# Kernel optimization log

Hardware: AMD Instinct MI355X
Metric: run time of the kernel (lower is better)

Reference implementation:

```python
import jax, jax.numpy as jnp
import numpy as np

N, M, E, C_IN, C_OUT = 100000, 20000, 1600000, 128, 128


def _safe_inv(d):
    # 1/d with 0 where d==0 (matches PyG D[D==inf]=0), grad-safe
    safe = jnp.where(d > 0, d, 1.0)
    return jnp.where(d > 0, 1.0 / safe, 0.0)


def _hconv(x, node_idx, edge_idx, hw, W, b):
    # PyG HypergraphConv, use_attention=False, heads=1:
    # X' = D^{-1} H B^{-1} H^T (X Theta) + bias, D uses hyperedge_weight
    xt = x @ W  # [N, C_OUT]
    D = jax.ops.segment_sum(hw[edge_idx], node_idx, num_segments=N)
    Dinv = _safe_inv(D)  # [N]
    Bc = jax.ops.segment_sum(jnp.ones((E,), dtype=x.dtype), edge_idx, num_segments=M)
    Binv = _safe_inv(Bc)  # [M]
    # node -> hyperedge (message weighted by B^{-1} of target edge)
    e = jax.ops.segment_sum(Binv[edge_idx][:, None] * xt[node_idx], edge_idx, num_segments=M)
    # hyperedge -> node (message weighted by D^{-1} of target node)
    out = jax.ops.segment_sum(Dinv[node_idx][:, None] * e[edge_idx], node_idx, num_segments=N)
    return out + b


def setup_inputs() -> dict:
    key = jax.random.key(0)
    ks = jax.random.split(key, 12)
    x = jax.random.normal(ks[0], (N, C_IN), dtype=jnp.float32)
    node_idx = jax.random.randint(ks[1], (E,), 0, N, dtype=jnp.int32)
    edge_idx = jax.random.randint(ks[2], (E,), 0, M, dtype=jnp.int32)
    hyperedge_index = jnp.stack([node_idx, edge_idx])
    hyperedge_weight = jax.random.uniform(ks[3], (M,), dtype=jnp.float32) + 0.5
    hyperedge_attr = jax.random.normal(ks[4], (M, C_IN), dtype=jnp.float32)
    batch = jnp.zeros((N,), dtype=jnp.int32)
    s1 = 1.0 / np.sqrt(C_IN)
    s2 = 1.0 / np.sqrt(C_OUT)
    W1 = jax.random.uniform(ks[5], (C_IN, C_OUT), minval=-s1, maxval=s1, dtype=jnp.float32)
    W2 = jax.random.uniform(ks[6], (C_OUT, C_OUT), minval=-s2, maxval=s2, dtype=jnp.float32)
    W3 = jax.random.uniform(ks[7], (C_OUT, C_OUT), minval=-s2, maxval=s2, dtype=jnp.float32)
    b1 = jax.random.uniform(ks[8], (C_OUT,), minval=-s1, maxval=s1, dtype=jnp.float32)
    b2 = jax.random.uniform(ks[9], (C_OUT,), minval=-s2, maxval=s2, dtype=jnp.float32)
    b3 = jax.random.uniform(ks[10], (C_OUT,), minval=-s2, maxval=s2, dtype=jnp.float32)
    return {"x": x, "hyperedge_index": hyperedge_index, "hyperedge_weight": hyperedge_weight,
            "hyperedge_attr": hyperedge_attr, "batch": batch,
            "W1": W1, "b1": b1, "W2": W2, "b2": b2, "W3": W3, "b3": b3}


def reference(x, hyperedge_index, hyperedge_weight, hyperedge_attr, batch,
              W1, b1, W2, b2, W3, b3):
    node_idx = hyperedge_index[0]
    edge_idx = hyperedge_index[1]
    # dropout is identity in eval mode; hyperedge_attr/batch unused (no attention)
    h = jax.nn.relu(_hconv(x, node_idx, edge_idx, hyperedge_weight, W1, b1))
    h = jax.nn.relu(_hconv(h, node_idx, edge_idx, hyperedge_weight, W2, b2))
    h = jax.nn.relu(_hconv(h, node_idx, edge_idx, hyperedge_weight, W3, b3))
    return h
```

## Files before the change

kernel.cpp:

```cpp
#include <hip/hip_runtime.h>
#include <hip/hip_fp16.h>

#define NN 100000
#define MM 20000
#define EE 1600000

#define NBLK_E 256
#define CHUNK_E (EE / NBLK_E)
#define NBLK_N 128
#define CHUNK_N (EE / NBLK_N)
#define NRANGE 25000

#define SCAN_BLOCK 256
#define SCAN_ITEMS 8
#define SCAN_TILE (SCAN_BLOCK * SCAN_ITEMS)
#define NB_E ((MM + SCAN_TILE - 1) / SCAN_TILE)
#define NB_N ((NN + SCAN_TILE - 1) / SCAN_TILE)
#define NB_TOT (NB_E + NB_N)

static inline size_t align256(size_t x) { return (x + 255) & ~(size_t)255; }

struct alignas(8) half4 { __half2 lo, hi; };

__device__ __forceinline__ float4 h4_to_f4(half4 v) {
  float2 a = __half22float2(v.lo);
  float2 b = __half22float2(v.hi);
  return make_float4(a.x, a.y, b.x, b.y);
}
__device__ __forceinline__ half4 f4_to_h4(float4 v) {
  half4 r;
  r.lo = __float22half2_rn(make_float2(v.x, v.y));
  r.hi = __float22half2_rn(make_float2(v.z, v.w));
  return r;
}

__global__ __launch_bounds__(256) void cvt_f2h_kernel(
    const float* __restrict__ in, __half* __restrict__ out, int n4) {
  int i = blockIdx.x * 256 + threadIdx.x;
  int stride = gridDim.x * 256;
  for (; i < n4; i += stride) {
    float4 v = ((const float4*)in)[i];
    ((half4*)out)[i] = f4_to_h4(v);
  }
}

__global__ __launch_bounds__(256) void ehist_kernel(
    const int* __restrict__ edge_idx,
    int* __restrict__ bcnt_e, unsigned short* __restrict__ lrank_e) {
  extern __shared__ int hist[];
  int b = blockIdx.x;
  for (int k = threadIdx.x; k < MM; k += 256) hist[k] = 0;
  __syncthreads();
  int lo = b * CHUNK_E, hi = lo + CHUNK_E;
  for (int i = lo + threadIdx.x; i < hi; i += 256) {
    int e = edge_idx[i];
    int r = atomicAdd(&hist[e], 1);
    lrank_e[i] = (unsigned short)r;
  }
  __syncthreads();
  int* row = bcnt_e + (size_t)b * MM;
  for (int k = threadIdx.x; k < MM; k += 256) row[k] = hist[k];
}

__global__ __launch_bounds__(256) void nhist_kernel(
    const int* __restrict__ node_idx,
    int* __restrict__ bcnt_n, unsigned short* __restrict__ lrank_n) {
  extern __shared__ int hist[];
  int b = blockIdx.x;
  int lo = b * CHUNK_N, hi = lo + CHUNK_N;
  int* row = bcnt_n + (size_t)b * NN;
  for (int p = 0; p < 4; ++p) {
    int base = p * NRANGE;
    for (int k = threadIdx.x; k < NRANGE; k += 256) hist[k] = 0;
    __syncthreads();
    for (int i = lo + threadIdx.x; i < hi; i += 256) {
      int n = node_idx[i] - base;
      if ((unsigned)n < (unsigned)NRANGE) {
        int r = atomicAdd(&hist[n], 1);
        lrank_n[i] = (unsigned short)r;
      }
    }
    __syncthreads();
    for (int k = threadIdx.x; k < NRANGE; k += 256) row[base + k] = hist[k];
    __syncthreads();
  }
}

__global__ __launch_bounds__(256) void colscan_e_kernel(
    int* __restrict__ bcnt_e, int* __restrict__ ecnt) {
  int e = blockIdx.x * 256 + threadIdx.x;
  if (e >= MM) return;
  int run = 0;
#pragma unroll 8
  for (int b = 0; b < NBLK_E; ++b) {
    size_t idx = (size_t)b * MM + e;
    int v = bcnt_e[idx];
    bcnt_e[idx] = run;
    run += v;
  }
  ecnt[e] = run;
}

__global__ __launch_bounds__(256) void colscan_n_kernel(
    int* __restrict__ bcnt_n, int* __restrict__ ncnt) {
  int n = blockIdx.x * 256 + threadIdx.x;
  if (n >= NN) return;
  int run = 0;
#pragma unroll 8
  for (int b = 0; b < NBLK_N; ++b) {
    size_t idx = (size_t)b * NN + n;
    int v = bcnt_n[idx];
    bcnt_n[idx] = run;
    run += v;
  }
  ncnt[n] = run;
}

__global__ __launch_bounds__(SCAN_BLOCK) void scan_partial_kernel(
    const int* __restrict__ ecnt, const int* __restrict__ ncnt,
    int* __restrict__ eptr, int* __restrict__ nptr, int* __restrict__ bsum) {
  __shared__ int lds[SCAN_BLOCK];
  int b = blockIdx.x;
  const int* cnt; int* ptr; int len; int lb;
  if (b < NB_E) { cnt = ecnt; ptr = eptr; len = MM; lb = b; }
  else          { cnt = ncnt; ptr = nptr; len = NN; lb = b - NB_E; }
  int t = threadIdx.x;
  int lo = lb * SCAN_TILE + t * SCAN_ITEMS;
  int v[SCAN_ITEMS];
  int s = 0;
#pragma unroll
  for (int j = 0; j < SCAN_ITEMS; ++j) {
    int idx = lo + j;
    v[j] = (idx < len) ? cnt[idx] : 0;
    s += v[j];
  }
  lds[t] = s;
  __syncthreads();
  for (int d = 1; d < SCAN_BLOCK; d <<= 1) {
    int o = (t >= d) ? lds[t - d] : 0;
    __syncthreads();
    lds[t] += o;
    __syncthreads();
  }
  int run = lds[t] - s;
#pragma unroll
  for (int j = 0; j < SCAN_ITEMS; ++j) {
    int idx = lo + j;
    if (idx < len) ptr[idx] = run;
    run += v[j];
  }
  if (t == SCAN_BLOCK - 1) bsum[b] = lds[t];
}

__global__ void scan_bsum_kernel(int* __restrict__ bsum) {
  int t = threadIdx.x;
  if (t == 0) {
    int run = 0;
    for (int i = 0; i < NB_E; ++i) { int c = bsum[i]; bsum[i] = run; run += c; }
  } else if (t == 1) {
    int run = 0;
    for (int i = NB_E; i < NB_TOT; ++i) { int c = bsum[i]; bsum[i] = run; run += c; }
  }
}

__global__ __launch_bounds__(SCAN_BLOCK) void scan_fixup_kernel(
    int* __restrict__ eptr, int* __restrict__ nptr,
    const int* __restrict__ ecnt, const int* __restrict__ bsum,
    float* __restrict__ Binv) {
  int b = blockIdx.x;
  int* ptr; int len; int lb; bool isE;
  if (b < NB_E) { ptr = eptr; len = MM; lb = b; isE = true; }
  else          { ptr = nptr; len = NN; lb = b - NB_E; isE = false; }
  int boff = bsum[b];
  int t = threadIdx.x;
  int lo = lb * SCAN_TILE + t * SCAN_ITEMS;
#pragma unroll
  for (int j = 0; j < SCAN_ITEMS; ++j) {
    int idx = lo + j;
    if (idx < len) {
      ptr[idx] += boff;
      if (isE) {
        int c = ecnt[idx];
        Binv[idx] = (c > 0) ? 1.0f / (float)c : 0.0f;
      }
    }
  }
  if (b == 0 && t == 0) { eptr[MM] = EE; nptr[NN] = EE; }
}

__global__ __launch_bounds__(256) void fill2_kernel(
    const int* __restrict__ node_idx, const int* __restrict__ edge_idx,
    const int* __restrict__ eptr, const int* __restrict__ nptr,
    const int* __restrict__ bcnt_e, const int* __restrict__ bcnt_n,
    const unsigned short* __restrict__ lrank_e,
    const unsigned short* __restrict__ lrank_n,
    int* __restrict__ edge_nodes, int* __restrict__ node_edges) {
  int i = blockIdx.x * 256 + threadIdx.x;
  if (i >= EE) return;
  int e = edge_idx[i];
  int n = node_idx[i];
  int be = i / CHUNK_E;
  int bn = i / CHUNK_N;
  int slotE = eptr[e] + bcnt_e[(size_t)be * MM + e] + (int)lrank_e[i];
  edge_nodes[slotE] = n;
  int slotN = nptr[n] + bcnt_n[(size_t)bn * NN + n] + (int)lrank_n[i];
  node_edges[slotN] = e;
}

__global__ __launch_bounds__(256) void dinv_csr_kernel(
    const int* __restrict__ nptr, const int* __restrict__ node_edges,
    const float* __restrict__ hw, float* __restrict__ Dinv) {
  int n = blockIdx.x * 256 + threadIdx.x;
  if (n >= NN) return;
  int lo = nptr[n], hi = nptr[n + 1];
  float d = 0.0f;
  for (int j = lo; j < hi; ++j) d += hw[node_edges[j]];
  Dinv[n] = (d > 0.0f) ? 1.0f / d : 0.0f;
}

__device__ __forceinline__ void fma4(float4& acc, float s, const float4& m) {
  acc.x += s * m.x;
  acc.y += s * m.y;
  acc.z += s * m.z;
  acc.w += s * m.w;
}

__global__ __launch_bounds__(256) void gemm128_kernel(
    const __half* __restrict__ X, const float* __restrict__ W,
    __half* __restrict__ Y, int nrows) {
  __shared__ float Wl[128 * 128];
  float4* Wl4 = (float4*)Wl;
  const float4* W4 = (const float4*)W;
  for (int i = threadIdx.x; i < 128 * 32; i += 256) Wl4[i] = W4[i];
  __syncthreads();

  int tc = threadIdx.x & 15;
  int tr = threadIdx.x >> 4;
  int base = blockIdx.x * 64;
  int r[4];
  bool v[4];
#pragma unroll
  for (int j = 0; j < 4; ++j) {
    int rr = base + tr + j * 16;
    v[j] = rr < nrows;
    r[j] = v[j] ? rr : 0;
  }
  float4 acc[4][2];
#pragma unroll
  for (int j = 0; j < 4; ++j) {
    acc[j][0] = make_float4(0.f, 0.f, 0.f, 0.f);
    acc[j][1] = make_float4(0.f, 0.f, 0.f, 0.f);
  }
#pragma unroll 4
  for (int k4 = 0; k4 < 32; ++k4) {
    float4 xv[4];
#pragma unroll
    for (int j = 0; j < 4; ++j)
      xv[j] = h4_to_f4(((const half4*)X)[(size_t)r[j] * 32 + k4]);
#pragma unroll
    for (int kk = 0; kk < 4; ++kk) {
      float4 wva = Wl4[(k4 * 4 + kk) * 32 + tc];
      float4 wvb = Wl4[(k4 * 4 + kk) * 32 + 16 + tc];
#pragma unroll
      for (int j = 0; j < 4; ++j) {
        float xk = ((const float*)&xv[j])[kk];
        fma4(acc[j][0], xk, wva);
        fma4(acc[j][1], xk, wvb);
      }
    }
  }
#pragma unroll
  for (int j = 0; j < 4; ++j) {
    if (v[j]) {
      ((half4*)Y)[(size_t)r[j] * 32 + tc] = f4_to_h4(acc[j][0]);
      ((half4*)Y)[(size_t)r[j] * 32 + 16 + tc] = f4_to_h4(acc[j][1]);
    }
  }
}

__global__ __launch_bounds__(256) void edge_agg_kernel(
    const __half* __restrict__ hin, const int* __restrict__ eptr,
    const int* __restrict__ edge_nodes, const float* __restrict__ Binv,
    __half* __restrict__ eout) {
  int half_id = threadIdx.x >> 5;
  int lane = threadIdx.x & 31;
  int m = blockIdx.x * 8 + half_id;
  if (m >= MM) return;
  int lo = eptr[m], hi = eptr[m + 1];
  const half4* h4p = (const half4*)hin;
  float4 acc = make_float4(0.f, 0.f, 0.f, 0.f);
  int j = lo;
  for (; j + 4 <= hi; j += 4) {
    int n0 = edge_nodes[j + 0];
    int n1 = edge_nodes[j + 1];
    int n2 = edge_nodes[j + 2];
    int n3 = edge_nodes[j + 3];
    float4 a = h4_to_f4(h4p[(size_t)n0 * 32 + lane]);
    float4 b = h4_to_f4(h4p[(size_t)n1 * 32 + lane]);
    float4 c = h4_to_f4(h4p[(size_t)n2 * 32 + lane]);
    float4 d = h4_to_f4(h4p[(size_t)n3 * 32 + lane]);
    acc.x += (a.x + b.x) + (c.x + d.x);
    acc.y += (a.y + b.y) + (c.y + d.y);
    acc.z += (a.z + b.z) + (c.z + d.z);
    acc.w += (a.w + b.w) + (c.w + d.w);
  }
  for (; j < hi; ++j) {
    int n = edge_nodes[j];
    float4 a = h4_to_f4(h4p[(size_t)n * 32 + lane]);
    acc.x += a.x; acc.y += a.y; acc.z += a.z; acc.w += a.w;
  }
  float bi = Binv[m];
  acc.x *= bi; acc.y *= bi; acc.z *= bi; acc.w *= bi;
  ((half4*)eout)[(size_t)m * 32 + lane] = f4_to_h4(acc);
}

__device__ __forceinline__ void strow(float* Y, size_t i, float4 v) {
  ((float4*)Y)[i] = v;
}
__device__ __forceinline__ void strow(__half* Y, size_t i, float4 v) {
  ((half4*)Y)[i] = f4_to_h4(v);
}

template <typename TOUT>
__global__ __launch_bounds__(256) void node_agg_kernel(
    const __half* __restrict__ ein, const int* __restrict__ nptr,
    const int* __restrict__ node_edges, const float* __restrict__ Dinv,
    const float* __restrict__ bias, TOUT* __restrict__ out) {
  int half_id = threadIdx.x >> 5;
  int lane = threadIdx.x & 31;
  int n = blockIdx.x * 8 + half_id;
  if (n >= NN) return;
  int lo = nptr[n], hi = nptr[n + 1];
  const half4* e4 = (const half4*)ein;
  float4 acc = make_float4(0.f, 0.f, 0.f, 0.f);
  int j = lo;
  for (; j + 4 <= hi; j += 4) {
    int m0 = node_edges[j + 0];
    int m1 = node_edges[j + 1];
    int m2 = node_edges[j + 2];
    int m3 = node_edges[j + 3];
    float4 a = h4_to_f4(e4[(size_t)m0 * 32 + lane]);
    float4 b = h4_to_f4(e4[(size_t)m1 * 32 + lane]);
    float4 c = h4_to_f4(e4[(size_t)m2 * 32 + lane]);
    float4 d = h4_to_f4(e4[(size_t)m3 * 32 + lane]);
    acc.x += (a.x + b.x) + (c.x + d.x);
    acc.y += (a.y + b.y) + (c.y + d.y);
    acc.z += (a.z + b.z) + (c.z + d.z);
    acc.w += (a.w + b.w) + (c.w + d.w);
  }
  for (; j < hi; ++j) {
    int m = node_edges[j];
    float4 a = h4_to_f4(e4[(size_t)m * 32 + lane]);
    acc.x += a.x; acc.y += a.y; acc.z += a.z; acc.w += a.w;
  }
  float di = Dinv[n];
  float4 bb = ((const float4*)bias)[lane];
  float4 rv;
  rv.x = fmaxf(di * acc.x + bb.x, 0.f);
  rv.y = fmaxf(di * acc.y + bb.y, 0.f);
  rv.z = fmaxf(di * acc.z + bb.z, 0.f);
  rv.w = fmaxf(di * acc.w + bb.w, 0.f);
  strow(out, (size_t)n * 32 + lane, rv);
}

extern "C" void kernel_launch(void* const* d_in, const int* in_sizes, int n_in,
                              void* d_out, int out_size, void* d_ws, size_t ws_size,
                              hipStream_t stream) {
  const float* x = (const float*)d_in[0];
  const int* hidx = (const int*)d_in[1];
  const int* node_idx = hidx;
  const int* edge_idx = hidx + EE;
  const float* hw = (const float*)d_in[2];
  const float* W1 = (const float*)d_in[5];
  const float* b1 = (const float*)d_in[6];
  const float* W2 = (const float*)d_in[7];
  const float* b2 = (const float*)d_in[8];
  const float* W3 = (const float*)d_in[9];
  const float* b3 = (const float*)d_in[10];
  float* out = (float*)d_out;

  char* ws = (char*)d_ws;
  size_t off = 0;
  auto alloc = [&](size_t bytes) -> char* {
    char* p = ws + off;
    off = align256(off + bytes);
    return p;
  };
  __half* xh   = (__half*)alloc(sizeof(__half) * (size_t)NN * 128);
  __half* h    = (__half*)alloc(sizeof(__half) * (size_t)NN * 128);
  __half* eraw = (__half*)alloc(sizeof(__half) * (size_t)MM * 128);
  __half* et   = (__half*)alloc(sizeof(__half) * (size_t)MM * 128);
  int*   bcnt_e = (int*)alloc(sizeof(int) * (size_t)NBLK_E * MM);
  int*   bcnt_n = (int*)alloc(sizeof(int) * (size_t)NBLK_N * NN);
  unsigned short* lrank_e = (unsigned short*)alloc(sizeof(short) * (size_t)EE);
  unsigned short* lrank_n = (unsigned short*)alloc(sizeof(short) * (size_t)EE);
  int*   ecnt  = (int*)alloc(sizeof(int) * MM);
  int*   ncnt  = (int*)alloc(sizeof(int) * NN);
  int*   eptr  = (int*)alloc(sizeof(int) * (MM + 1));
  int*   nptr  = (int*)alloc(sizeof(int) * (NN + 1));
  int*   bsum  = (int*)alloc(sizeof(int) * NB_TOT);
  float* Binv  = (float*)alloc(sizeof(float) * MM);
  float* Dinv  = (float*)alloc(sizeof(float) * NN);
  int* edge_nodes = (int*)alloc(sizeof(int) * (size_t)EE);
  int* node_edges = (int*)alloc(sizeof(int) * (size_t)EE);
  (void)ws_size; (void)in_sizes; (void)n_in; (void)out_size;

  ehist_kernel<<<NBLK_E, 256, MM * sizeof(int), stream>>>(edge_idx, bcnt_e, lrank_e);
  nhist_kernel<<<NBLK_N, 256, NRANGE * sizeof(int), stream>>>(node_idx, bcnt_n, lrank_n);
  colscan_e_kernel<<<(MM + 255) / 256, 256, 0, stream>>>(bcnt_e, ecnt);
  colscan_n_kernel<<<(NN + 255) / 256, 256, 0, stream>>>(bcnt_n, ncnt);
  scan_partial_kernel<<<NB_TOT, SCAN_BLOCK, 0, stream>>>(ecnt, ncnt, eptr, nptr, bsum);
  scan_bsum_kernel<<<1, 64, 0, stream>>>(bsum);
  scan_fixup_kernel<<<NB_TOT, SCAN_BLOCK, 0, stream>>>(eptr, nptr, ecnt, bsum, Binv);
  fill2_kernel<<<(EE + 255) / 256, 256, 0, stream>>>(node_idx, edge_idx, eptr, nptr,
                                                     bcnt_e, bcnt_n, lrank_e, lrank_n,
                                                     edge_nodes, node_edges);
  dinv_csr_kernel<<<(NN + 255) / 256, 256, 0, stream>>>(nptr, node_edges, hw, Dinv);
  cvt_f2h_kernel<<<1024, 256, 0, stream>>>(x, xh, NN * 32);

  const int gemmE_grid = (MM + 63) / 64;
  const int eagg_grid = MM / 8;
  const int nagg_grid = NN / 8;

  edge_agg_kernel<<<eagg_grid, 256, 0, stream>>>(xh, eptr, edge_nodes, Binv, eraw);
  gemm128_kernel<<<gemmE_grid, 256, 0, stream>>>(eraw, W1, et, MM);
  node_agg_kernel<__half><<<nagg_grid, 256, 0, stream>>>(et, nptr, node_edges,
                                                         Dinv, b1, h);
  edge_agg_kernel<<<eagg_grid, 256, 0, stream>>>(h, eptr, edge_nodes, Binv, eraw);
  gemm128_kernel<<<gemmE_grid, 256, 0, stream>>>(eraw, W2, et, MM);
  node_agg_kernel<__half><<<nagg_grid, 256, 0, stream>>>(et, nptr, node_edges,
                                                         Dinv, b2, xh);
  edge_agg_kernel<<<eagg_grid, 256, 0, stream>>>(xh, eptr, edge_nodes, Binv, eraw);
  gemm128_kernel<<<gemmE_grid, 256, 0, stream>>>(eraw, W3, et, MM);
  node_agg_kernel<float><<<nagg_grid, 256, 0, stream>>>(et, nptr, node_edges,
                                                        Dinv, b3, out);
}
```

Baseline: 628.9 us.

## Shrink histogram counts to 16-bit, merge colscans, split node aggregation by column halves

```diff
diff --git a/kernel.cpp b/kernel.cpp
--- a/kernel.cpp
+++ b/kernel.cpp
@@ -9,7 +9,7 @@
 #define CHUNK_E (EE / NBLK_E)
 #define NBLK_N 128
 #define CHUNK_N (EE / NBLK_N)
-#define NRANGE 25000
+#define NRANGE2 50000
 
 #define SCAN_BLOCK 256
 #define SCAN_ITEMS 8
@@ -46,7 +46,7 @@
 
 __global__ __launch_bounds__(256) void ehist_kernel(
     const int* __restrict__ edge_idx,
-    int* __restrict__ bcnt_e, unsigned short* __restrict__ lrank_e) {
+    unsigned short* __restrict__ bcnt_e, unsigned short* __restrict__ lrank_e) {
   extern __shared__ int hist[];
   int b = blockIdx.x;
   for (int k = threadIdx.x; k < MM; k += 256) hist[k] = 0;
@@ -58,62 +58,72 @@
     lrank_e[i] = (unsigned short)r;
   }
   __syncthreads();
-  int* row = bcnt_e + (size_t)b * MM;
-  for (int k = threadIdx.x; k < MM; k += 256) row[k] = hist[k];
+  unsigned short* row = bcnt_e + (size_t)b * MM;
+  for (int k = threadIdx.x; k < MM / 2; k += 256) {
+    ushort2 w;
+    w.x = (unsigned short)hist[2 * k];
+    w.y = (unsigned short)hist[2 * k + 1];
+    ((ushort2*)row)[k] = w;
+  }
 }
 
 __global__ __launch_bounds__(256) void nhist_kernel(
     const int* __restrict__ node_idx,
-    int* __restrict__ bcnt_n, unsigned short* __restrict__ lrank_n) {
-  extern __shared__ int hist[];
+    unsigned short* __restrict__ bcnt_n, unsigned short* __restrict__ lrank_n) {
+  extern __shared__ unsigned int histp[];
   int b = blockIdx.x;
   int lo = b * CHUNK_N, hi = lo + CHUNK_N;
-  int* row = bcnt_n + (size_t)b * NN;
-  for (int p = 0; p < 4; ++p) {
-    int base = p * NRANGE;
-    for (int k = threadIdx.x; k < NRANGE; k += 256) hist[k] = 0;
+  unsigned short* row = bcnt_n + (size_t)b * NN;
+  for (int p = 0; p < 2; ++p) {
+    int base = p * NRANGE2;
+    for (int k = threadIdx.x; k < NRANGE2 / 2; k += 256) histp[k] = 0;
     __syncthreads();
     for (int i = lo + threadIdx.x; i < hi; i += 256) {
       int n = node_idx[i] - base;
-      if ((unsigned)n < (unsigned)NRANGE) {
-        int r = atomicAdd(&hist[n], 1);
-        lrank_n[i] = (unsigned short)r;
+      if ((unsigned)n < (unsigned)NRANGE2) {
+        unsigned add = (n & 1) ? 0x10000u : 1u;
+        unsigned old = atomicAdd(&histp[n >> 1], add);
+        lrank_n[i] = (unsigned short)((old >> ((n & 1) * 16)) & 0xFFFFu);
       }
     }
     __syncthreads();
-    for (int k = threadIdx.x; k < NRANGE; k += 256) row[base + k] = hist[k];
+    for (int k = threadIdx.x; k < NRANGE2 / 2; k += 256) {
+      unsigned w = histp[k];
+      ushort2 o;
+      o.x = (unsigned short)(w & 0xFFFFu);
+      o.y = (unsigned short)(w >> 16);
+      ((ushort2*)(row + base))[k] = o;
+    }
     __syncthreads();
   }
 }
 
-__global__ __launch_bounds__(256) void colscan_e_kernel(
-    int* __restrict__ bcnt_e, int* __restrict__ ecnt) {
-  int e = blockIdx.x * 256 + threadIdx.x;
-  if (e >= MM) return;
-  int run = 0;
+__global__ __launch_bounds__(256) void colscan_kernel(
+    unsigned short* __restrict__ bcnt_e, unsigned short* __restrict__ bcnt_n,
+    int* __restrict__ ecnt, int* __restrict__ ncnt) {
+  int i = blockIdx.x * 256 + threadIdx.x;
+  if (i < MM) {
+    int run = 0;
 #pragma unroll 8
-  for (int b = 0; b < NBLK_E; ++b) {
-    size_t idx = (size_t)b * MM + e;
-    int v = bcnt_e[idx];
-    bcnt_e[idx] = run;
-    run += v;
-  }
-  ecnt[e] = run;
-}
-
-__global__ __launch_bounds__(256) void colscan_n_kernel(
-    int* __restrict__ bcnt_n, int* __restrict__ ncnt) {
-  int n = blockIdx.x * 256 + threadIdx.x;
-  if (n >= NN) return;
-  int run = 0;
+    for (int b = 0; b < NBLK_E; ++b) {
+      size_t idx = (size_t)b * MM + i;
+      int v = bcnt_e[idx];
+      bcnt_e[idx] = (unsigned short)run;
+      run += v;
+    }
+    ecnt[i] = run;
+  } else if (i < MM + NN) {
+    int n = i - MM;
+    int run = 0;
 #pragma unroll 8
-  for (int b = 0; b < NBLK_N; ++b) {
-    size_t idx = (size_t)b * NN + n;
-    int v = bcnt_n[idx];
-    bcnt_n[idx] = run;
-    run += v;
-  }
-  ncnt[n] = run;
+    for (int b = 0; b < NBLK_N; ++b) {
+      size_t idx = (size_t)b * NN + n;
+      int v = bcnt_n[idx];
+      bcnt_n[idx] = (unsigned short)run;
+      run += v;
+    }
+    ncnt[n] = run;
+  }
 }
 
 __global__ __launch_bounds__(SCAN_BLOCK) void scan_partial_kernel(
@@ -191,7 +201,8 @@
 __global__ __launch_bounds__(256) void fill2_kernel(
     const int* __restrict__ node_idx, const int* __restrict__ edge_idx,
     const int* __restrict__ eptr, const int* __restrict__ nptr,
-    const int* __restrict__ bcnt_e, const int* __restrict__ bcnt_n,
+    const unsigned short* __restrict__ bcnt_e,
+    const unsigned short* __restrict__ bcnt_n,
     const unsigned short* __restrict__ lrank_e,
     const unsigned short* __restrict__ lrank_n,
     int* __restrict__ edge_nodes, int* __restrict__ node_edges) {
@@ -201,9 +212,9 @@
   int n = node_idx[i];
   int be = i / CHUNK_E;
   int bn = i / CHUNK_N;
-  int slotE = eptr[e] + bcnt_e[(size_t)be * MM + e] + (int)lrank_e[i];
+  int slotE = eptr[e] + (int)bcnt_e[(size_t)be * MM + e] + (int)lrank_e[i];
   edge_nodes[slotE] = n;
-  int slotN = nptr[n] + bcnt_n[(size_t)bn * NN + n] + (int)lrank_n[i];
+  int slotN = nptr[n] + (int)bcnt_n[(size_t)bn * NN + n] + (int)lrank_n[i];
   node_edges[slotN] = e;
 }
 
@@ -290,19 +301,17 @@
   const half4* h4p = (const half4*)hin;
   float4 acc = make_float4(0.f, 0.f, 0.f, 0.f);
   int j = lo;
-  for (; j + 4 <= hi; j += 4) {
-    int n0 = edge_nodes[j + 0];
-    int n1 = edge_nodes[j + 1];
-    int n2 = edge_nodes[j + 2];
-    int n3 = edge_nodes[j + 3];
-    float4 a = h4_to_f4(h4p[(size_t)n0 * 32 + lane]);
-    float4 b = h4_to_f4(h4p[(size_t)n1 * 32 + lane]);
-    float4 c = h4_to_f4(h4p[(size_t)n2 * 32 + lane]);
-    float4 d = h4_to_f4(h4p[(size_t)n3 * 32 + lane]);
-    acc.x += (a.x + b.x) + (c.x + d.x);
-    acc.y += (a.y + b.y) + (c.y + d.y);
-    acc.z += (a.z + b.z) + (c.z + d.z);
-    acc.w += (a.w + b.w) + (c.w + d.w);
+  for (; j + 8 <= hi; j += 8) {
+    int idx[8];
+#pragma unroll
+    for (int u = 0; u < 8; ++u) idx[u] = edge_nodes[j + u];
+    float4 s[8];
+#pragma unroll
+    for (int u = 0; u < 8; ++u) s[u] = h4_to_f4(h4p[(size_t)idx[u] * 32 + lane]);
+    acc.x += ((s[0].x + s[1].x) + (s[2].x + s[3].x)) + ((s[4].x + s[5].x) + (s[6].x + s[7].x));
+    acc.y += ((s[0].y + s[1].y) + (s[2].y + s[3].y)) + ((s[4].y + s[5].y) + (s[6].y + s[7].y));
+    acc.z += ((s[0].z + s[1].z) + (s[2].z + s[3].z)) + ((s[4].z + s[5].z) + (s[6].z + s[7].z));
+    acc.w += ((s[0].w + s[1].w) + (s[2].w + s[3].w)) + ((s[4].w + s[5].w) + (s[6].w + s[7].w));
   }
   for (; j < hi; ++j) {
     int n = edge_nodes[j];
@@ -314,22 +323,22 @@
   ((half4*)eout)[(size_t)m * 32 + lane] = f4_to_h4(acc);
 }
 
-__device__ __forceinline__ void strow(float* Y, size_t i, float4 v) {
-  ((float4*)Y)[i] = v;
-}
-__device__ __forceinline__ void strow(__half* Y, size_t i, float4 v) {
-  ((half4*)Y)[i] = f4_to_h4(v);
+__device__ __forceinline__ void strow_q(float* Y, size_t row, int q, float4 v) {
+  ((float4*)Y)[row * 32 + q] = v;
+}
+__device__ __forceinline__ void strow_q(__half* Y, size_t row, int q, float4 v) {
+  ((half4*)Y)[row * 32 + q] = f4_to_h4(v);
 }
 
 template <typename TOUT>
-__global__ __launch_bounds__(256) void node_agg_kernel(
+__global__ __launch_bounds__(256) void node_agg_half_kernel(
     const __half* __restrict__ ein, const int* __restrict__ nptr,
     const int* __restrict__ node_edges, const float* __restrict__ Dinv,
-    const float* __restrict__ bias, TOUT* __restrict__ out) {
-  int half_id = threadIdx.x >> 5;
-  int lane = threadIdx.x & 31;
-  int n = blockIdx.x * 8 + half_id;
-  if (n >= NN) return;
+    const float* __restrict__ bias, TOUT* __restrict__ out, int c4) {
+  int g = threadIdx.x >> 4;
+  int gl = threadIdx.x & 15;
+  int n = blockIdx.x * 16 + g;
+  int q = c4 + gl;
   int lo = nptr[n], hi = nptr[n + 1];
   const half4* e4 = (const half4*)ein;
   float4 acc = make_float4(0.f, 0.f, 0.f, 0.f);
@@ -339,10 +348,10 @@
     int m1 = node_edges[j + 1];
     int m2 = node_edges[j + 2];
     int m3 = node_edges[j + 3];
-    float4 a = h4_to_f4(e4[(size_t)m0 * 32 + lane]);
-    float4 b = h4_to_f4(e4[(size_t)m1 * 32 + lane]);
-    float4 c = h4_to_f4(e4[(size_t)m2 * 32 + lane]);
-    float4 d = h4_to_f4(e4[(size_t)m3 * 32 + lane]);
+    float4 a = h4_to_f4(e4[(size_t)m0 * 32 + q]);
+    float4 b = h4_to_f4(e4[(size_t)m1 * 32 + q]);
+    float4 c = h4_to_f4(e4[(size_t)m2 * 32 + q]);
+    float4 d = h4_to_f4(e4[(size_t)m3 * 32 + q]);
     acc.x += (a.x + b.x) + (c.x + d.x);
     acc.y += (a.y + b.y) + (c.y + d.y);
     acc.z += (a.z + b.z) + (c.z + d.z);
@@ -350,17 +359,17 @@
   }
   for (; j < hi; ++j) {
     int m = node_edges[j];
-    float4 a = h4_to_f4(e4[(size_t)m * 32 + lane]);
+    float4 a = h4_to_f4(e4[(size_t)m * 32 + q]);
     acc.x += a.x; acc.y += a.y; acc.z += a.z; acc.w += a.w;
   }
   float di = Dinv[n];
-  float4 bb = ((const float4*)bias)[lane];
+  float4 bb = ((const float4*)bias)[q];
   float4 rv;
   rv.x = fmaxf(di * acc.x + bb.x, 0.f);
   rv.y = fmaxf(di * acc.y + bb.y, 0.f);
   rv.z = fmaxf(di * acc.z + bb.z, 0.f);
   rv.w = fmaxf(di * acc.w + bb.w, 0.f);
-  strow(out, (size_t)n * 32 + lane, rv);
+  strow_q(out, (size_t)n, q, rv);
 }
 
 extern "C" void kernel_launch(void* const* d_in, const int* in_sizes, int n_in,
@@ -390,8 +399,8 @@
   __half* h    = (__half*)alloc(sizeof(__half) * (size_t)NN * 128);
   __half* eraw = (__half*)alloc(sizeof(__half) * (size_t)MM * 128);
   __half* et   = (__half*)alloc(sizeof(__half) * (size_t)MM * 128);
-  int*   bcnt_e = (int*)alloc(sizeof(int) * (size_t)NBLK_E * MM);
-  int*   bcnt_n = (int*)alloc(sizeof(int) * (size_t)NBLK_N * NN);
+  unsigned short* bcnt_e = (unsigned short*)alloc(sizeof(short) * (size_t)NBLK_E * MM);
+  unsigned short* bcnt_n = (unsigned short*)alloc(sizeof(short) * (size_t)NBLK_N * NN);
   unsigned short* lrank_e = (unsigned short*)alloc(sizeof(short) * (size_t)EE);
   unsigned short* lrank_n = (unsigned short*)alloc(sizeof(short) * (size_t)EE);
   int*   ecnt  = (int*)alloc(sizeof(int) * MM);
@@ -406,9 +415,8 @@
   (void)ws_size; (void)in_sizes; (void)n_in; (void)out_size;
 
   ehist_kernel<<<NBLK_E, 256, MM * sizeof(int), stream>>>(edge_idx, bcnt_e, lrank_e);
-  nhist_kernel<<<NBLK_N, 256, NRANGE * sizeof(int), stream>>>(node_idx, bcnt_n, lrank_n);
-  colscan_e_kernel<<<(MM + 255) / 256, 256, 0, stream>>>(bcnt_e, ecnt);
-  colscan_n_kernel<<<(NN + 255) / 256, 256, 0, stream>>>(bcnt_n, ncnt);
+  nhist_kernel<<<NBLK_N, 256, (NRANGE2 / 2) * sizeof(int), stream>>>(node_idx, bcnt_n, lrank_n);
+  colscan_kernel<<<(MM + NN + 255) / 256, 256, 0, stream>>>(bcnt_e, bcnt_n, ecnt, ncnt);
   scan_partial_kernel<<<NB_TOT, SCAN_BLOCK, 0, stream>>>(ecnt, ncnt, eptr, nptr, bsum);
   scan_bsum_kernel<<<1, 64, 0, stream>>>(bsum);
   scan_fixup_kernel<<<NB_TOT, SCAN_BLOCK, 0, stream>>>(eptr, nptr, ecnt, bsum, Binv);
@@ -420,18 +428,18 @@
 
   const int gemmE_grid = (MM + 63) / 64;
   const int eagg_grid = MM / 8;
-  const int nagg_grid = NN / 8;
+  const int nagg_grid = NN / 16;
 
   edge_agg_kernel<<<eagg_grid, 256, 0, stream>>>(xh, eptr, edge_nodes, Binv, eraw);
   gemm128_kernel<<<gemmE_grid, 256, 0, stream>>>(eraw, W1, et, MM);
-  node_agg_kernel<__half><<<nagg_grid, 256, 0, stream>>>(et, nptr, node_edges,
-                                                         Dinv, b1, h);
+  node_agg_half_kernel<__half><<<nagg_grid, 256, 0, stream>>>(et, nptr, node_edges, Dinv, b1, h, 0);
+  node_agg_half_kernel<__half><<<nagg_grid, 256, 0, stream>>>(et, nptr, node_edges, Dinv, b1, h, 16);
   edge_agg_kernel<<<eagg_grid, 256, 0, stream>>>(h, eptr, edge_nodes, Binv, eraw);
   gemm128_kernel<<<gemmE_grid, 256, 0, stream>>>(eraw, W2, et, MM);
-  node_agg_kernel<__half><<<nagg_grid, 256, 0, stream>>>(et, nptr, node_edges,
-                                                         Dinv, b2, xh);
+  node_agg_half_kernel<__half><<<nagg_grid, 256, 0, stream>>>(et, nptr, node_edges, Dinv, b2, xh, 0);
+  node_agg_half_kernel<__half><<<nagg_grid, 256, 0, stream>>>(et, nptr, node_edges, Dinv, b2, xh, 16);
   edge_agg_kernel<<<eagg_grid, 256, 0, stream>>>(xh, eptr, edge_nodes, Binv, eraw);
   gemm128_kernel<<<gemmE_grid, 256, 0, stream>>>(eraw, W3, et, MM);
-  node_agg_kernel<float><<<nagg_grid, 256, 0, stream>>>(et, nptr, node_edges,
-                                                        Dinv, b3, out);
-}
+  node_agg_half_kernel<float><<<nagg_grid, 256, 0, stream>>>(et, nptr, node_edges, Dinv, b3, out, 0);
+  node_agg_half_kernel<float><<<nagg_grid, 256, 0, stream>>>(et, nptr, node_edges, Dinv, b3, out, 16);
+}
```

After: 600.3 us. 1.05x faster.
